# Kernel tuning notes

Measured on AMD Instinct MI355X. Metric: run time of the kernel, lower is better.

Reference implementation:

```python
import jax, jax.numpy as jnp
import numpy as np

H = 512      # hidden_size
R = 47       # response_size
TR = 2       # treat_size
B = 128
T = 512


def _uniform(key, shape, k):
    return jax.random.uniform(key, shape, jnp.float32, -k, k)


def setup_inputs() -> dict:
    key = jax.random.key(0)
    ks = jax.random.split(key, 20)
    kinit = 1.0 / np.sqrt(H)
    inp = {
        "x_r": jax.random.normal(ks[0], (B, T, R), jnp.float32),
        "x_t": jax.random.normal(ks[1], (B, T, TR), jnp.float32),
        # r_rnn: 2-layer LSTM, input size R+TR=49 (torch gate order i,f,g,o)
        "r_Wih0": _uniform(ks[2], (4 * H, R + TR), kinit),
        "r_Whh0": _uniform(ks[3], (4 * H, H), kinit),
        "r_b0": _uniform(ks[4], (4 * H,), kinit),  # b_ih + b_hh fused
        "r_Wih1": _uniform(ks[5], (4 * H, H), kinit),
        "r_Whh1": _uniform(ks[6], (4 * H, H), kinit),
        "r_b1": _uniform(ks[7], (4 * H,), kinit),
        # t_rnn: 2-layer LSTM, input size 2*R+TR=96
        "t_Wih0": _uniform(ks[8], (4 * H, 2 * R + TR), kinit),
        "t_Whh0": _uniform(ks[9], (4 * H, H), kinit),
        "t_b0": _uniform(ks[10], (4 * H,), kinit),
        "t_Wih1": _uniform(ks[11], (4 * H, H), kinit),
        "t_Whh1": _uniform(ks[12], (4 * H, H), kinit),
        "t_b1": _uniform(ks[13], (4 * H,), kinit),
        # output linears
        "Wr": _uniform(ks[14], (R, H), kinit),
        "br": _uniform(ks[15], (R,), kinit),
        "Wt": _uniform(ks[16], (TR, H), kinit),
        "bt": _uniform(ks[17], (TR,), kinit),
    }
    return inp


def _lstm_cell(x, h, c, Wih, Whh, b):
    gates = x @ Wih.T + h @ Whh.T + b          # [B, 4H]
    i, f, g, o = jnp.split(gates, 4, axis=-1)
    c = jax.nn.sigmoid(f) * c + jax.nn.sigmoid(i) * jnp.tanh(g)
    h = jax.nn.sigmoid(o) * jnp.tanh(c)
    return h, c


def reference(x_r, x_t, r_Wih0, r_Whh0, r_b0, r_Wih1, r_Whh1, r_b1,
              t_Wih0, t_Whh0, t_b0, t_Wih1, t_Whh1, t_b1, Wr, br, Wt, bt):
    b = x_r.shape[0]
    z = jnp.zeros((b, H), x_r.dtype)
    carry0 = (z, z, z, z, z, z, z, z)  # (h,c) for 2 layers of r_rnn and t_rnn

    def step(carry, rt):
        hr0, cr0, hr1, cr1, ht0, ct0, ht1, ct1 = carry
        r, t = rt
        r_input = jnp.concatenate([r, t], axis=-1)          # [B, 49]
        hr0, cr0 = _lstm_cell(r_input, hr0, cr0, r_Wih0, r_Whh0, r_b0)
        hr1, cr1 = _lstm_cell(hr0, hr1, cr1, r_Wih1, r_Whh1, r_b1)
        r_out = hr1 @ Wr.T + br                             # [B, 47]
        t_input = jnp.concatenate([r_input, r_out], axis=-1)  # [B, 96]
        ht0, ct0 = _lstm_cell(t_input, ht0, ct0, t_Wih0, t_Whh0, t_b0)
        ht1, ct1 = _lstm_cell(ht0, ht1, ct1, t_Wih1, t_Whh1, t_b1)
        t_out = ht1 @ Wt.T + bt                             # [B, 2]
        return (hr0, cr0, hr1, cr1, ht0, ct0, ht1, ct1), (r_out, t_out)

    xs = (jnp.swapaxes(x_r, 0, 1), jnp.swapaxes(x_t, 0, 1))  # time-major [T,B,.]
    _, (r_seq, t_seq) = jax.lax.scan(step, carry0, xs)
    # back to batch-first, like the module's final permute(1,0,2)
    return jnp.swapaxes(r_seq, 0, 1), jnp.swapaxes(t_seq, 0, 1)
```

## Files before the change

### kernel.cpp

```cpp
#include <hip/hip_runtime.h>


typedef _Float16 half_t;
typedef _Float16 half8 __attribute__((ext_vector_type(8)));
typedef float floatx4 __attribute__((ext_vector_type(4)));
typedef unsigned long long ull_t;

#define OFF_W0 0
#define OFF_W1 131072
#define OFF_W2 1179648
#define OFF_W3 2228224
#define OFF_W4 3276800
#define OFF_W5 3407872
#define OFF_W6 3538944
#define OFF_W7 4587520
#define OFF_W8 5636096
#define OFF_W9 6684672
#define OFF_W10 6709248
#define W_TOTAL 6717440
#define H_BASE  6717440
#define RO_BASE 7241728
#define HALF_TOTAL 7258112
#define STATE_BYTE_OFF (H_BASE * 2)
#define C_BYTE_OFF (HALF_TOTAL * 2)
#define BAR_BYTE_OFF 15564800
#define X16_BYTE_OFF (BAR_BYTE_OFF + 4096)
#define WS_NEED_X16 ((unsigned long long)X16_BYTE_OFF + 8388608ull)
#define STATE_BYTES (X16_BYTE_OFF - STATE_BYTE_OFF)

#define NBLK 256
#define TOUT_BASE (128 * 512 * 47)

__device__ __forceinline__ floatx4 mfma16(half8 a, half8 b, floatx4 c) {
  return __builtin_amdgcn_mfma_f32_16x16x32_f16(a, b, c, 0, 0, 0);
}
__device__ __forceinline__ float fast_sig(float x) {
  x = fminf(fmaxf(x, -30.f), 30.f);
  float e = __expf(-x);
  return __builtin_amdgcn_rcpf(1.f + e);
}
__device__ __forceinline__ float fast_tanh(float x) {
  x = fminf(fmaxf(x, -15.f), 15.f);
  float e = __expf(-2.f * x);
  return (1.f - e) * __builtin_amdgcn_rcpf(1.f + e);
}

template <int N>
__device__ __forceinline__ void coh_stage(half8 (&bb)[N], const half_t* p) {
#pragma unroll
  for (int ks = 0; ks < N; ++ks)
    asm volatile("global_load_dwordx4 %0, %1, off sc0 sc1"
                 : "=v"(bb[ks]) : "v"(p + ks * 32));
}
__device__ __forceinline__ void drain_vm() {
  asm volatile("s_waitcnt vmcnt(0)" ::: "memory");
  __builtin_amdgcn_sched_barrier(0);
}
__device__ __forceinline__ void store_h4_coh(half_t* p, half_t h0, half_t h1,
                                             half_t h2, half_t h3) {
  union { ull_t u; _Float16 h[4]; } x;
  x.h[0] = h0; x.h[1] = h1; x.h[2] = h2; x.h[3] = h3;
  __hip_atomic_store((ull_t*)p, x.u, __ATOMIC_RELAXED,
                     __HIP_MEMORY_SCOPE_AGENT);
}
template <int PACE>
__device__ __forceinline__ void poll_llc(const unsigned* p, unsigned target) {
  for (;;) {
    unsigned v;
    asm volatile("global_load_dword %0, %1, off sc0 sc1\ns_waitcnt vmcnt(0)"
                 : "=v"(v) : "v"(p));
    if (v >= target) return;
    __builtin_amdgcn_s_sleep(PACE);
  }
}

__device__ __forceinline__ void slab_issue(half8 (&tmp)[4],
                                           const half_t* __restrict__ src,
                                           int tid) {
#pragma unroll
  for (int j = 0; j < 4; ++j) {
    const int u = tid + j * 256;
    asm volatile("global_load_dwordx4 %0, %1, off sc0 sc1"
                 : "=v"(tmp[j]) : "v"(src + (u >> 6) * 512 + (u & 63) * 8));
  }
}
__device__ __forceinline__ void slab_write(char* base, const half8 (&tmp)[4],
                                           int tid) {
#pragma unroll
  for (int j = 0; j < 4; ++j) {
    const int u = tid + j * 256;
    const int row = u >> 6, seg = u & 63;
    *(half8*)(base + row * 1024 + ((seg * 16) ^ ((row & 7) << 4))) = tmp[j];
  }
}

template <int NT, int NSEG, int LDW>
__device__ __forceinline__ void gemm_lb(const half_t* __restrict__ W,
                                        const int* wrow, const char* ldsb,
                                        int lk, int q, int l15,
                                        floatx4 (&acc)[NT]) {
  const int bbase = l15 * 1024;
  const int bxor = (l15 & 7) << 4;
#pragma unroll
  for (int ks = 0; ks < NSEG; ++ks) {
    const int kb = ks * 32 + lk;
    half8 b = *(const half8*)(ldsb + bbase + ((q * 16 + ks * 64) ^ bxor));
#pragma unroll
    for (int n = 0; n < NT; ++n) {
      half8 a = *(const half8*)(W + (long)(wrow[n] + l15) * LDW + kb);
      acc[n] = mfma16(a, b, acc[n]);
    }
  }
}

template <int NT, int NSEG, int LDW>
__device__ __forceinline__ void gemm_regB(const half_t* __restrict__ W,
                                          const int* wrow,
                                          const half8 (&bb)[NSEG], int lk,
                                          int l15, floatx4 (&acc)[NT]) {
#pragma unroll
  for (int ks = 0; ks < NSEG; ++ks) {
    const int kb = ks * 32 + lk;
#pragma unroll
    for (int n = 0; n < NT; ++n) {
      half8 a = *(const half8*)(W + (long)(wrow[n] + l15) * LDW + kb);
      acc[n] = mfma16(a, bb[ks], acc[n]);
    }
  }
}

__device__ __forceinline__ void gemm_x16(const half_t* __restrict__ W,
                                         const int* wrow,
                                         const half_t* __restrict__ xb, int lk,
                                         int l15, floatx4 (&acc)[4]) {
#pragma unroll
  for (int ks = 0; ks < 2; ++ks) {
    const int kb = ks * 32 + lk;
    half8 b = *(const half8*)(xb + kb);
#pragma unroll
    for (int n = 0; n < 4; ++n) {
      half8 a = *(const half8*)(W + (long)(wrow[n] + l15) * 64 + kb);
      acc[n] = mfma16(a, b, acc[n]);
    }
  }
}
__device__ __forceinline__ void gemm_xf(const float* __restrict__ xr,
                                        const float* __restrict__ xt, int t,
                                        int batch, const half_t* __restrict__ W,
                                        const int* wrow, int lk, int l15,
                                        floatx4 (&acc)[4]) {
#pragma unroll
  for (int ks = 0; ks < 2; ++ks) {
    const int kb = ks * 32 + lk;
    half8 b;
    const long base = (long)batch * 512 + t;
#pragma unroll
    for (int j = 0; j < 8; ++j) {
      const int kk = kb + j;
      float f = 0.f;
      if (kk < 47) f = xr[base * 47 + kk];
      else if (kk < 49) f = xt[base * 2 + (kk - 47)];
      b[j] = (half_t)f;
    }
#pragma unroll
    for (int n = 0; n < 4; ++n) {
      half8 a = *(const half8*)(W + (long)(wrow[n] + l15) * 64 + kb);
      acc[n] = mfma16(a, b, acc[n]);
    }
  }
}

__device__ __forceinline__ void lstm_epi_sw(floatx4 (&acc)[4],
                                            const float* __restrict__ bias,
                                            float* __restrict__ cst,
                                            half_t* __restrict__ hdst,
                                            int batch, int hcol0) {
  const floatx4 bI = *(const floatx4*)(bias + hcol0);
  const floatx4 bF = *(const floatx4*)(bias + 512 + hcol0);
  const floatx4 bG = *(const floatx4*)(bias + 1024 + hcol0);
  const floatx4 bO = *(const floatx4*)(bias + 1536 + hcol0);
  const int off = batch * 512 + hcol0;
  floatx4 cold = *(floatx4*)(cst + off);
  floatx4 cn;
  half_t hn[4];
#pragma unroll
  for (int r = 0; r < 4; ++r) {
    const float gi = acc[0][r] + bI[r];
    const float gf = acc[1][r] + bF[r];
    const float gg = acc[2][r] + bG[r];
    const float go = acc[3][r] + bO[r];
    cn[r] = fast_sig(gf) * cold[r] + fast_sig(gi) * fast_tanh(gg);
    hn[r] = (half_t)(fast_sig(go) * fast_tanh(cn[r]));
  }
  *(floatx4*)(cst + off) = cn;
  store_h4_coh(hdst + off, hn[0], hn[1], hn[2], hn[3]);
}

__global__ __launch_bounds__(256, 1) void adrnn_persist(
    const float* __restrict__ xr, const float* __restrict__ xt,
    const float* __restrict__ b_r0, const float* __restrict__ b_r1,
    const float* __restrict__ b_t0, const float* __restrict__ b_t1,
    const float* __restrict__ brv, const float* __restrict__ btv,
    half_t* __restrict__ w16, float* __restrict__ cbase,
    float* __restrict__ out, unsigned* bar, const half_t* __restrict__ x16,
    int use_x16) {
  __shared__ half8 lds_v[2048];
  char* lds0 = (char*)lds_v;
  char* lds1 = lds0 + 16384;

  const int bid = blockIdx.x;
  const int tid = threadIdx.x;
  const int lane = tid & 63;
  const int w = tid >> 6;
  const int l15 = lane & 15;
  const int q = lane >> 4;
  const int lk = q * 8;
  half_t* H = w16 + H_BASE;
  half_t* RO = w16 + RO_BASE;
#define HB(cell, p) (H + (((cell)*2 + (p)) << 16))

  const int stage = (bid & 7) >> 1;
  const int hgHi = bid & 1;
  const int rr = bid >> 3;
  const int hgLo = rr >> 3;
  const int bg = rr & 7;
  const int hg = hgHi * 4 + hgLo;
  const int c0w = hg * 64 + w * 16;
  const int b0 = bg * 16;
  const int batch = b0 + l15;
  const int hcol0 = c0w + q * 4;
  const int sd = (stage == 0) ? 0 : (stage == 1) ? 1 : (stage == 2) ? 3 : 4;
  int wrow[4] = {c0w, 512 + c0w, 1024 + c0w, 1536 + c0w};
  const int flat = (hg * 8 + bg) * 4 + w;
  const bool is_spare = (stage == 0 && hg < 2 && flat < 32);

  unsigned* larr = bar + (bid & 7) * 32;
  unsigned* garr = bar + 256;
  unsigned* lgen = bar + 288 + (bid & 7) * 32;

  for (int k = 0; k < 517; ++k) {
    const int par = k & 1, pq = par ^ 1;
    const int t = k - sd;
    const bool valid = (t >= 0 && t < 512);

    if (valid) {
      half8 s0[4], s1[4];
      if (stage == 0) {
        slab_issue(s0, HB(0, pq) + b0 * 512, tid);
        drain_vm();
        slab_write(lds0, s0, tid);
      } else if (stage == 1) {
        slab_issue(s0, HB(0, pq) + b0 * 512, tid);
        slab_issue(s1, HB(1, pq) + b0 * 512, tid);
        drain_vm();
        slab_write(lds0, s0, tid);
        slab_write(lds1, s1, tid);
      } else if (stage == 2) {
        slab_issue(s0, HB(2, pq) + b0 * 512, tid);
        drain_vm();
        slab_write(lds0, s0, tid);
      } else {
        slab_issue(s0, HB(2, pq) + b0 * 512, tid);
        slab_issue(s1, HB(3, pq) + b0 * 512, tid);
        drain_vm();
        slab_write(lds0, s0, tid);
        slab_write(lds1, s1, tid);
      }
    }
    __syncthreads();

    if (valid) {
      floatx4 acc[4] = {};
      if (stage == 0) {
        if (use_x16)
          gemm_x16(w16 + OFF_W0, wrow, x16 + (long)t * 8192 + batch * 64, lk, l15, acc);
        else
          gemm_xf(xr, xt, t, batch, w16 + OFF_W0, wrow, lk, l15, acc);
        gemm_lb<4, 16, 512>(w16 + OFF_W1, wrow, lds0, lk, q, l15, acc);
        lstm_epi_sw(acc, b_r0, cbase + 0 * 65536, HB(0, par), batch, hcol0);
      } else if (stage == 1) {
        gemm_lb<4, 16, 512>(w16 + OFF_W2, wrow, lds0, lk, q, l15, acc);
        gemm_lb<4, 16, 512>(w16 + OFF_W3, wrow, lds1, lk, q, l15, acc);
        lstm_epi_sw(acc, b_r1, cbase + 1 * 65536, HB(1, par), batch, hcol0);
      } else if (stage == 2) {
        half8 bro[2];
        coh_stage<2>(bro, RO + pq * 8192 + batch * 64 + lk);
        drain_vm();
        if (use_x16)
          gemm_x16(w16 + OFF_W4, wrow, x16 + (long)t * 8192 + batch * 64, lk, l15, acc);
        else
          gemm_xf(xr, xt, t, batch, w16 + OFF_W4, wrow, lk, l15, acc);
        gemm_regB<4, 2, 64>(w16 + OFF_W5, wrow, bro, lk, l15, acc);
        gemm_lb<4, 16, 512>(w16 + OFF_W6, wrow, lds0, lk, q, l15, acc);
        lstm_epi_sw(acc, b_t0, cbase + 2 * 65536, HB(2, par), batch, hcol0);
      } else {
        gemm_lb<4, 16, 512>(w16 + OFF_W7, wrow, lds0, lk, q, l15, acc);
        gemm_lb<4, 16, 512>(w16 + OFF_W8, wrow, lds1, lk, q, l15, acc);
        lstm_epi_sw(acc, b_t1, cbase + 3 * 65536, HB(3, par), batch, hcol0);
      }
    }

    if (is_spare) {
      if (flat < 24) {
        const int tr = k - 2;
        if (tr >= 0 && tr < 512) {
          const int n = flat >> 3, btl = flat & 7;
          const int rb = btl * 16 + l15;
          half8 bs[16];
          coh_stage<16>(bs, HB(1, pq) + rb * 512 + lk);
          drain_vm();
          int wr1[1] = {n * 16};
          floatx4 accr[1] = {};
          gemm_regB<1, 16, 512>(w16 + OFF_W9, wr1, bs, lk, l15, accr);
          const int wc0 = n * 16 + q * 4;
          half_t ro4[4];
#pragma unroll
          for (int r = 0; r < 4; ++r) {
            const int wc = wc0 + r;
            float v = 0.f;
            if (wc < 47) {
              v = accr[0][r] + brv[wc];
              out[((long)rb * 512 + tr) * 47 + wc] = v;
            }
            ro4[r] = (half_t)v;
          }
          store_h4_coh(RO + par * 8192 + rb * 64 + wc0, ro4[0], ro4[1], ro4[2], ro4[3]);
        }
      } else {
        const int tt = k - 5;
        if (tt >= 0 && tt < 512) {
          const int btl = flat - 24;
          const int rb = btl * 16 + l15;
          half8 bs[16];
          coh_stage<16>(bs, HB(3, pq) + rb * 512 + lk);
          drain_vm();
          int wt1[1] = {0};
          floatx4 accw[1] = {};
          gemm_regB<1, 16, 512>(w16 + OFF_W10, wt1, bs, lk, l15, accw);
          if (q == 0) {
#pragma unroll
            for (int r = 0; r < 2; ++r)
              out[TOUT_BASE + ((long)rb * 512 + tt) * 2 + r] = accw[0][r] + btv[r];
          }
        }
      }
    }

    asm volatile("s_waitcnt vmcnt(0)" ::: "memory");
    __syncthreads();
    if (tid == 0) {
      const unsigned ku = (unsigned)k + 1u;
      (void)__hip_atomic_fetch_add(larr, 1u, __ATOMIC_RELAXED,
                                   __HIP_MEMORY_SCOPE_AGENT);
      if (bid < 8) {
        poll_llc<1>(larr, 32u * ku);
        (void)__hip_atomic_fetch_add(garr, 1u, __ATOMIC_RELAXED,
                                     __HIP_MEMORY_SCOPE_AGENT);
        poll_llc<1>(garr, 8u * ku);
        (void)__hip_atomic_fetch_add(lgen, 1u, __ATOMIC_RELAXED,
                                     __HIP_MEMORY_SCOPE_AGENT);
      } else {
        poll_llc<3>(lgen, ku);
      }
    }
    __syncthreads();
    asm volatile("" ::: "memory");
  }
#undef HB
}

__global__ __launch_bounds__(256) void conv_w(
    const float* __restrict__ rWih0, const float* __restrict__ rWhh0,
    const float* __restrict__ rWih1, const float* __restrict__ rWhh1,
    const float* __restrict__ tWih0, const float* __restrict__ tWhh0,
    const float* __restrict__ tWih1, const float* __restrict__ tWhh1,
    const float* __restrict__ Wr, const float* __restrict__ Wt,
    half_t* __restrict__ w16) {
  const int idx = blockIdx.x * 256 + threadIdx.x;
  if (idx >= W_TOTAL) return;
  float v = 0.f;
  if (idx < OFF_W1) {
    int n = idx >> 6, kk = idx & 63;
    if (kk < 49) v = rWih0[n * 49 + kk];
  } else if (idx < OFF_W2) {
    int r = idx - OFF_W1; v = rWhh0[r];
  } else if (idx < OFF_W3) {
    int r = idx - OFF_W2; v = rWih1[r];
  } else if (idx < OFF_W4) {
    int r = idx - OFF_W3; v = rWhh1[r];
  } else if (idx < OFF_W5) {
    int r = idx - OFF_W4; int n = r >> 6, kk = r & 63;
    if (kk < 49) v = tWih0[n * 96 + kk];
  } else if (idx < OFF_W6) {
    int r = idx - OFF_W5; int n = r >> 6, kk = r & 63;
    if (kk < 47) v = tWih0[n * 96 + 49 + kk];
  } else if (idx < OFF_W7) {
    int r = idx - OFF_W6; v = tWhh0[r];
  } else if (idx < OFF_W8) {
    int r = idx - OFF_W7; v = tWih1[r];
  } else if (idx < OFF_W9) {
    int r = idx - OFF_W8; v = tWhh1[r];
  } else if (idx < OFF_W10) {
    int r = idx - OFF_W9; int n = r >> 9, kk = r & 511;
    if (n < 47) v = Wr[n * 512 + kk];
  } else {
    int r = idx - OFF_W10; int n = r >> 9, kk = r & 511;
    if (n < 2) v = Wt[n * 512 + kk];
  }
  w16[idx] = (half_t)v;
}

__global__ __launch_bounds__(256) void conv_x(const float* __restrict__ xr,
                                              const float* __restrict__ xt,
                                              half_t* __restrict__ x16) {
  const int idx = blockIdx.x * 256 + threadIdx.x;
  if (idx >= 512 * 128 * 64) return;
  const int kk = idx & 63;
  const int row = (idx >> 6) & 127;
  const int t = idx >> 13;
  float v = 0.f;
  if (kk < 47) v = xr[(row * 512 + t) * 47 + kk];
  else if (kk < 49) v = xt[(row * 512 + t) * 2 + (kk - 47)];
  x16[idx] = (half_t)v;
}

extern "C" void kernel_launch(void* const* d_in, const int* in_sizes, int n_in,
                              void* d_out, int out_size, void* d_ws,
                              size_t ws_size, hipStream_t stream) {
  const float* xr = (const float*)d_in[0];
  const float* xt = (const float*)d_in[1];
  const float* rWih0 = (const float*)d_in[2];
  const float* rWhh0 = (const float*)d_in[3];
  const float* r_b0 = (const float*)d_in[4];
  const float* rWih1 = (const float*)d_in[5];
  const float* rWhh1 = (const float*)d_in[6];
  const float* r_b1 = (const float*)d_in[7];
  const float* tWih0 = (const float*)d_in[8];
  const float* tWhh0 = (const float*)d_in[9];
  const float* t_b0 = (const float*)d_in[10];
  const float* tWih1 = (const float*)d_in[11];
  const float* tWhh1 = (const float*)d_in[12];
  const float* t_b1 = (const float*)d_in[13];
  const float* Wr = (const float*)d_in[14];
  const float* br = (const float*)d_in[15];
  const float* Wt = (const float*)d_in[16];
  const float* bt = (const float*)d_in[17];

  half_t* w16 = (half_t*)d_ws;
  float* cbase = (float*)((char*)d_ws + C_BYTE_OFF);
  unsigned* bar = (unsigned*)((char*)d_ws + BAR_BYTE_OFF);
  half_t* x16 = (half_t*)((char*)d_ws + X16_BYTE_OFF);
  float* out = (float*)d_out;
  int use_x16 = (ws_size >= WS_NEED_X16) ? 1 : 0;

  (void)hipMemsetAsync((char*)d_ws + STATE_BYTE_OFF, 0, STATE_BYTES, stream);

  conv_w<<<(W_TOTAL + 255) / 256, 256, 0, stream>>>(
      rWih0, rWhh0, rWih1, rWhh1, tWih0, tWhh0, tWih1, tWhh1, Wr, Wt, w16);
  if (use_x16)
    conv_x<<<(512 * 128 * 64) / 256, 256, 0, stream>>>(xr, xt, x16);

  adrnn_persist<<<NBLK, 256, 0, stream>>>(xr, xt, r_b0, r_b1, t_b0, t_b1, br,
                                          bt, w16, cbase, out, bar, x16,
                                          use_x16);
}
```

Measured before the change: 9.214 ms.

## Remap blocks so most hidden-state traffic stays XCD-local; publish cross-stage h via LLC

Changes the block-to-work mapping so the producer and consumer of each LSTM layer's hidden state share the same XCD (bid&1 parity). Those local exchanges now use non-system-coherent loads and plain stores. Only the cross-stage h (layer 0 to layer 1, t-layer 0 to t-layer 1) is written a second time to a separate global buffer with LLC-coherent stores. The output-projection spare work moves to stage-1 and stage-3 blocks that read locally, aiming to cut the latency of coherent memory traffic on every timestep, at the cost of a duplicate h store and some reliance on same-XCD L2 visibility.

```diff
diff --git a/kernel.cpp b/kernel.cpp
--- a/kernel.cpp
+++ b/kernel.cpp
@@ -20,10 +20,11 @@
 #define W_TOTAL 6717440
 #define H_BASE  6717440
 #define RO_BASE 7241728
-#define HALF_TOTAL 7258112
+#define HG_BASE 7258112
+#define HALF_END 7520256
 #define STATE_BYTE_OFF (H_BASE * 2)
-#define C_BYTE_OFF (HALF_TOTAL * 2)
-#define BAR_BYTE_OFF 15564800
+#define C_BYTE_OFF (HALF_END * 2)
+#define BAR_BYTE_OFF (C_BYTE_OFF + 1048576)
 #define X16_BYTE_OFF (BAR_BYTE_OFF + 4096)
 #define WS_NEED_X16 ((unsigned long long)X16_BYTE_OFF + 8388608ull)
 #define STATE_BYTES (X16_BYTE_OFF - STATE_BYTE_OFF)
@@ -46,22 +47,26 @@
 }
 
 template <int N>
-__device__ __forceinline__ void coh_stage(half8 (&bb)[N], const half_t* p) {
+__device__ __forceinline__ void burst_g(half8 (&bb)[N], const half_t* p) {
 #pragma unroll
   for (int ks = 0; ks < N; ++ks)
     asm volatile("global_load_dwordx4 %0, %1, off sc0 sc1"
                  : "=v"(bb[ks]) : "v"(p + ks * 32));
 }
+template <int N>
+__device__ __forceinline__ void burst_l(half8 (&bb)[N], const half_t* p) {
+#pragma unroll
+  for (int ks = 0; ks < N; ++ks)
+    asm volatile("global_load_dwordx4 %0, %1, off sc0"
+                 : "=v"(bb[ks]) : "v"(p + ks * 32));
+}
 __device__ __forceinline__ void drain_vm() {
   asm volatile("s_waitcnt vmcnt(0)" ::: "memory");
   __builtin_amdgcn_sched_barrier(0);
 }
-__device__ __forceinline__ void store_h4_coh(half_t* p, half_t h0, half_t h1,
-                                             half_t h2, half_t h3) {
-  union { ull_t u; _Float16 h[4]; } x;
-  x.h[0] = h0; x.h[1] = h1; x.h[2] = h2; x.h[3] = h3;
-  __hip_atomic_store((ull_t*)p, x.u, __ATOMIC_RELAXED,
-                     __HIP_MEMORY_SCOPE_AGENT);
+__device__ __forceinline__ void store8_llc(half_t* p, ull_t v) {
+  asm volatile("global_store_dwordx2 %0, %1, off sc0 sc1"
+               :: "v"(p), "v"(v) : "memory");
 }
 template <int PACE>
 __device__ __forceinline__ void poll_llc(const unsigned* p, unsigned target) {
@@ -74,14 +79,19 @@
   }
 }
 
+template <int LLC>
 __device__ __forceinline__ void slab_issue(half8 (&tmp)[4],
                                            const half_t* __restrict__ src,
                                            int tid) {
 #pragma unroll
   for (int j = 0; j < 4; ++j) {
     const int u = tid + j * 256;
-    asm volatile("global_load_dwordx4 %0, %1, off sc0 sc1"
-                 : "=v"(tmp[j]) : "v"(src + (u >> 6) * 512 + (u & 63) * 8));
+    if constexpr (LLC)
+      asm volatile("global_load_dwordx4 %0, %1, off sc0 sc1"
+                   : "=v"(tmp[j]) : "v"(src + (u >> 6) * 512 + (u & 63) * 8));
+    else
+      asm volatile("global_load_dwordx4 %0, %1, off sc0"
+                   : "=v"(tmp[j]) : "v"(src + (u >> 6) * 512 + (u & 63) * 8));
   }
 }
 __device__ __forceinline__ void slab_write(char* base, const half8 (&tmp)[4],
@@ -112,7 +122,6 @@
     }
   }
 }
-
 template <int NT, int NSEG, int LDW>
 __device__ __forceinline__ void gemm_regB(const half_t* __restrict__ W,
                                           const int* wrow,
@@ -128,7 +137,6 @@
     }
   }
 }
-
 __device__ __forceinline__ void gemm_x16(const half_t* __restrict__ W,
                                          const int* wrow,
                                          const half_t* __restrict__ xb, int lk,
@@ -170,11 +178,11 @@
   }
 }
 
-__device__ __forceinline__ void lstm_epi_sw(floatx4 (&acc)[4],
-                                            const float* __restrict__ bias,
-                                            float* __restrict__ cst,
-                                            half_t* __restrict__ hdst,
-                                            int batch, int hcol0) {
+__device__ __forceinline__ void lstm_epi(floatx4 (&acc)[4],
+                                         const float* __restrict__ bias,
+                                         float* __restrict__ cst,
+                                         half_t* __restrict__ hld,
+                                         half_t* hgd, int batch, int hcol0) {
   const floatx4 bI = *(const floatx4*)(bias + hcol0);
   const floatx4 bF = *(const floatx4*)(bias + 512 + hcol0);
   const floatx4 bG = *(const floatx4*)(bias + 1024 + hcol0);
@@ -182,7 +190,7 @@
   const int off = batch * 512 + hcol0;
   floatx4 cold = *(floatx4*)(cst + off);
   floatx4 cn;
-  half_t hn[4];
+  union { ull_t u; _Float16 h[4]; } pk;
 #pragma unroll
   for (int r = 0; r < 4; ++r) {
     const float gi = acc[0][r] + bI[r];
@@ -190,10 +198,11 @@
     const float gg = acc[2][r] + bG[r];
     const float go = acc[3][r] + bO[r];
     cn[r] = fast_sig(gf) * cold[r] + fast_sig(gi) * fast_tanh(gg);
-    hn[r] = (half_t)(fast_sig(go) * fast_tanh(cn[r]));
+    pk.h[r] = (half_t)(fast_sig(go) * fast_tanh(cn[r]));
   }
   *(floatx4*)(cst + off) = cn;
-  store_h4_coh(hdst + off, hn[0], hn[1], hn[2], hn[3]);
+  *(ull_t*)(hld + off) = pk.u;
+  if (hgd) store8_llc(hgd + off, pk.u);
 }
 
 __global__ __launch_bounds__(256, 1) void adrnn_persist(
@@ -215,24 +224,25 @@
   const int l15 = lane & 15;
   const int q = lane >> 4;
   const int lk = q * 8;
-  half_t* H = w16 + H_BASE;
+  half_t* HL = w16 + H_BASE;
   half_t* RO = w16 + RO_BASE;
-#define HB(cell, p) (H + (((cell)*2 + (p)) << 16))
+#define HLB(cell, s) (HL + (((cell)*2 + (s)) << 16))
+#define HG0(s) (w16 + HG_BASE + ((s) << 16))
+#define HG2(s) (w16 + HG_BASE + 131072 + ((s) << 16))
 
   const int stage = (bid & 7) >> 1;
-  const int hgHi = bid & 1;
-  const int rr = bid >> 3;
-  const int hgLo = rr >> 3;
-  const int bg = rr & 7;
-  const int hg = hgHi * 4 + hgLo;
+  const int p = bid & 1;
+  const int u = bid >> 3;
+  const int hg = u >> 2;
+  const int bgHi = u & 3;
+  const int bg = bgHi * 2 + p;
   const int c0w = hg * 64 + w * 16;
   const int b0 = bg * 16;
   const int batch = b0 + l15;
   const int hcol0 = c0w + q * 4;
   const int sd = (stage == 0) ? 0 : (stage == 1) ? 1 : (stage == 2) ? 3 : 4;
   int wrow[4] = {c0w, 512 + c0w, 1024 + c0w, 1536 + c0w};
-  const int flat = (hg * 8 + bg) * 4 + w;
-  const bool is_spare = (stage == 0 && hg < 2 && flat < 32);
+  const int flat = u * 4 + w;
 
   unsigned* larr = bar + (bid & 7) * 32;
   unsigned* garr = bar + 256;
@@ -246,22 +256,22 @@
     if (valid) {
       half8 s0[4], s1[4];
       if (stage == 0) {
-        slab_issue(s0, HB(0, pq) + b0 * 512, tid);
+        slab_issue<0>(s0, HLB(0, pq) + b0 * 512, tid);
         drain_vm();
         slab_write(lds0, s0, tid);
       } else if (stage == 1) {
-        slab_issue(s0, HB(0, pq) + b0 * 512, tid);
-        slab_issue(s1, HB(1, pq) + b0 * 512, tid);
+        slab_issue<1>(s0, HG0(pq) + b0 * 512, tid);
+        slab_issue<0>(s1, HLB(1, pq) + b0 * 512, tid);
         drain_vm();
         slab_write(lds0, s0, tid);
         slab_write(lds1, s1, tid);
       } else if (stage == 2) {
-        slab_issue(s0, HB(2, pq) + b0 * 512, tid);
+        slab_issue<0>(s0, HLB(2, pq) + b0 * 512, tid);
         drain_vm();
         slab_write(lds0, s0, tid);
       } else {
-        slab_issue(s0, HB(2, pq) + b0 * 512, tid);
-        slab_issue(s1, HB(3, pq) + b0 * 512, tid);
+        slab_issue<1>(s0, HG2(pq) + b0 * 512, tid);
+        slab_issue<0>(s1, HLB(3, pq) + b0 * 512, tid);
         drain_vm();
         slab_write(lds0, s0, tid);
         slab_write(lds1, s1, tid);
@@ -277,14 +287,14 @@
         else
           gemm_xf(xr, xt, t, batch, w16 + OFF_W0, wrow, lk, l15, acc);
         gemm_lb<4, 16, 512>(w16 + OFF_W1, wrow, lds0, lk, q, l15, acc);
-        lstm_epi_sw(acc, b_r0, cbase + 0 * 65536, HB(0, par), batch, hcol0);
+        lstm_epi(acc, b_r0, cbase + 0 * 65536, HLB(0, par), HG0(par), batch, hcol0);
       } else if (stage == 1) {
         gemm_lb<4, 16, 512>(w16 + OFF_W2, wrow, lds0, lk, q, l15, acc);
         gemm_lb<4, 16, 512>(w16 + OFF_W3, wrow, lds1, lk, q, l15, acc);
-        lstm_epi_sw(acc, b_r1, cbase + 1 * 65536, HB(1, par), batch, hcol0);
+        lstm_epi(acc, b_r1, cbase + 1 * 65536, HLB(1, par), nullptr, batch, hcol0);
       } else if (stage == 2) {
         half8 bro[2];
-        coh_stage<2>(bro, RO + pq * 8192 + batch * 64 + lk);
+        burst_g<2>(bro, RO + pq * 8192 + batch * 64 + lk);
         drain_vm();
         if (use_x16)
           gemm_x16(w16 + OFF_W4, wrow, x16 + (long)t * 8192 + batch * 64, lk, l15, acc);
@@ -292,56 +302,55 @@
           gemm_xf(xr, xt, t, batch, w16 + OFF_W4, wrow, lk, l15, acc);
         gemm_regB<4, 2, 64>(w16 + OFF_W5, wrow, bro, lk, l15, acc);
         gemm_lb<4, 16, 512>(w16 + OFF_W6, wrow, lds0, lk, q, l15, acc);
-        lstm_epi_sw(acc, b_t0, cbase + 2 * 65536, HB(2, par), batch, hcol0);
+        lstm_epi(acc, b_t0, cbase + 2 * 65536, HLB(2, par), HG2(par), batch, hcol0);
       } else {
         gemm_lb<4, 16, 512>(w16 + OFF_W7, wrow, lds0, lk, q, l15, acc);
         gemm_lb<4, 16, 512>(w16 + OFF_W8, wrow, lds1, lk, q, l15, acc);
-        lstm_epi_sw(acc, b_t1, cbase + 3 * 65536, HB(3, par), batch, hcol0);
+        lstm_epi(acc, b_t1, cbase + 3 * 65536, HLB(3, par), nullptr, batch, hcol0);
       }
     }
 
-    if (is_spare) {
-      if (flat < 24) {
-        const int tr = k - 2;
-        if (tr >= 0 && tr < 512) {
-          const int n = flat >> 3, btl = flat & 7;
-          const int rb = btl * 16 + l15;
-          half8 bs[16];
-          coh_stage<16>(bs, HB(1, pq) + rb * 512 + lk);
-          drain_vm();
-          int wr1[1] = {n * 16};
-          floatx4 accr[1] = {};
-          gemm_regB<1, 16, 512>(w16 + OFF_W9, wr1, bs, lk, l15, accr);
-          const int wc0 = n * 16 + q * 4;
-          half_t ro4[4];
-#pragma unroll
-          for (int r = 0; r < 4; ++r) {
-            const int wc = wc0 + r;
-            float v = 0.f;
-            if (wc < 47) {
-              v = accr[0][r] + brv[wc];
-              out[((long)rb * 512 + tr) * 47 + wc] = v;
-            }
-            ro4[r] = (half_t)v;
+    if (stage == 1 && flat < 12) {
+      const int tr = k - 2;
+      if (tr >= 0 && tr < 512) {
+        const int n = flat >> 2;
+        const int btl = (flat & 3) * 2 + p;
+        const int rb = btl * 16 + l15;
+        half8 bs[16];
+        burst_l<16>(bs, HLB(1, pq) + rb * 512 + lk);
+        drain_vm();
+        int wr1[1] = {n * 16};
+        floatx4 accr[1] = {};
+        gemm_regB<1, 16, 512>(w16 + OFF_W9, wr1, bs, lk, l15, accr);
+        const int wc0 = n * 16 + q * 4;
+        union { ull_t u2; _Float16 h[4]; } rp;
+#pragma unroll
+        for (int r = 0; r < 4; ++r) {
+          const int wc = wc0 + r;
+          float v = 0.f;
+          if (wc < 47) {
+            v = accr[0][r] + brv[wc];
+            out[((long)rb * 512 + tr) * 47 + wc] = v;
           }
-          store_h4_coh(RO + par * 8192 + rb * 64 + wc0, ro4[0], ro4[1], ro4[2], ro4[3]);
+          rp.h[r] = (half_t)v;
         }
-      } else {
-        const int tt = k - 5;
-        if (tt >= 0 && tt < 512) {
-          const int btl = flat - 24;
-          const int rb = btl * 16 + l15;
-          half8 bs[16];
-          coh_stage<16>(bs, HB(3, pq) + rb * 512 + lk);
-          drain_vm();
-          int wt1[1] = {0};
-          floatx4 accw[1] = {};
-          gemm_regB<1, 16, 512>(w16 + OFF_W10, wt1, bs, lk, l15, accw);
-          if (q == 0) {
-#pragma unroll
-            for (int r = 0; r < 2; ++r)
-              out[TOUT_BASE + ((long)rb * 512 + tt) * 2 + r] = accw[0][r] + btv[r];
-          }
+        store8_llc(RO + par * 8192 + rb * 64 + wc0, rp.u2);
+      }
+    } else if (stage == 3 && flat < 4) {
+      const int tt = k - 5;
+      if (tt >= 0 && tt < 512) {
+        const int btl = flat * 2 + p;
+        const int rb = btl * 16 + l15;
+        half8 bs[16];
+        burst_l<16>(bs, HLB(3, pq) + rb * 512 + lk);
+        drain_vm();
+        int wt1[1] = {0};
+        floatx4 accw[1] = {};
+        gemm_regB<1, 16, 512>(w16 + OFF_W10, wt1, bs, lk, l15, accw);
+        if (q == 0) {
+#pragma unroll
+          for (int r = 0; r < 2; ++r)
+            out[TOUT_BASE + ((long)rb * 512 + tt) * 2 + r] = accw[0][r] + btv[r];
         }
       }
     }
@@ -366,7 +375,9 @@
     __syncthreads();
     asm volatile("" ::: "memory");
   }
-#undef HB
+#undef HLB
+#undef HG0
+#undef HG2
 }
 
 __global__ __launch_bounds__(256) void conv_w(
```

After: 11.74 ms. 1.27x slower.

## Halve persistent blocks, double per-wave gate tiles, fold output heads into stages

Applied to the files above, without the earlier changes.

Cuts the persistent grid from 256 to 128 blocks. Each wave now computes two 16-column hidden tiles per gate, eight accumulators instead of four, so the LDS-staged hidden state is reused across twice as many weight rows. The separate spare blocks that computed the r_out and t_out linears are gone. Those projections now run in existing stage-1 and stage-3 blocks, which reuse the h already in LDS instead of reloading it from global memory. The barrier arrival count is lowered to match, which reduces synchronisation fan-in, at the cost of more serial MFMA and weight-load work per block each step.

```diff
diff --git a/kernel.cpp b/kernel.cpp
--- a/kernel.cpp
+++ b/kernel.cpp
@@ -28,7 +28,7 @@
 #define WS_NEED_X16 ((unsigned long long)X16_BYTE_OFF + 8388608ull)
 #define STATE_BYTES (X16_BYTE_OFF - STATE_BYTE_OFF)
 
-#define NBLK 256
+#define NBLK 128
 #define TOUT_BASE (128 * 512 * 47)
 
 __device__ __forceinline__ floatx4 mfma16(half8 a, half8 b, floatx4 c) {
@@ -46,7 +46,7 @@
 }
 
 template <int N>
-__device__ __forceinline__ void coh_stage(half8 (&bb)[N], const half_t* p) {
+__device__ __forceinline__ void burst_g(half8 (&bb)[N], const half_t* p) {
 #pragma unroll
   for (int ks = 0; ks < N; ++ks)
     asm volatile("global_load_dwordx4 %0, %1, off sc0 sc1"
@@ -56,12 +56,8 @@
   asm volatile("s_waitcnt vmcnt(0)" ::: "memory");
   __builtin_amdgcn_sched_barrier(0);
 }
-__device__ __forceinline__ void store_h4_coh(half_t* p, half_t h0, half_t h1,
-                                             half_t h2, half_t h3) {
-  union { ull_t u; _Float16 h[4]; } x;
-  x.h[0] = h0; x.h[1] = h1; x.h[2] = h2; x.h[3] = h3;
-  __hip_atomic_store((ull_t*)p, x.u, __ATOMIC_RELAXED,
-                     __HIP_MEMORY_SCOPE_AGENT);
+__device__ __forceinline__ void store_h4_coh(half_t* p, ull_t v) {
+  __hip_atomic_store((ull_t*)p, v, __ATOMIC_RELAXED, __HIP_MEMORY_SCOPE_AGENT);
 }
 template <int PACE>
 __device__ __forceinline__ void poll_llc(const unsigned* p, unsigned target) {
@@ -73,6 +69,10 @@
     __builtin_amdgcn_s_sleep(PACE);
   }
 }
+__device__ __forceinline__ void cnt_add(unsigned* p) {
+  (void)__hip_atomic_fetch_add(p, 1u, __ATOMIC_RELAXED,
+                               __HIP_MEMORY_SCOPE_AGENT);
+}
 
 __device__ __forceinline__ void slab_issue(half8 (&tmp)[4],
                                            const half_t* __restrict__ src,
@@ -112,7 +112,6 @@
     }
   }
 }
-
 template <int NT, int NSEG, int LDW>
 __device__ __forceinline__ void gemm_regB(const half_t* __restrict__ W,
                                           const int* wrow,
@@ -128,27 +127,28 @@
     }
   }
 }
-
+template <int NT>
 __device__ __forceinline__ void gemm_x16(const half_t* __restrict__ W,
                                          const int* wrow,
                                          const half_t* __restrict__ xb, int lk,
-                                         int l15, floatx4 (&acc)[4]) {
+                                         int l15, floatx4 (&acc)[NT]) {
 #pragma unroll
   for (int ks = 0; ks < 2; ++ks) {
     const int kb = ks * 32 + lk;
     half8 b = *(const half8*)(xb + kb);
 #pragma unroll
-    for (int n = 0; n < 4; ++n) {
+    for (int n = 0; n < NT; ++n) {
       half8 a = *(const half8*)(W + (long)(wrow[n] + l15) * 64 + kb);
       acc[n] = mfma16(a, b, acc[n]);
     }
   }
 }
+template <int NT>
 __device__ __forceinline__ void gemm_xf(const float* __restrict__ xr,
                                         const float* __restrict__ xt, int t,
                                         int batch, const half_t* __restrict__ W,
                                         const int* wrow, int lk, int l15,
-                                        floatx4 (&acc)[4]) {
+                                        floatx4 (&acc)[NT]) {
 #pragma unroll
   for (int ks = 0; ks < 2; ++ks) {
     const int kb = ks * 32 + lk;
@@ -163,37 +163,41 @@
       b[j] = (half_t)f;
     }
 #pragma unroll
-    for (int n = 0; n < 4; ++n) {
+    for (int n = 0; n < NT; ++n) {
       half8 a = *(const half8*)(W + (long)(wrow[n] + l15) * 64 + kb);
       acc[n] = mfma16(a, b, acc[n]);
     }
   }
 }
 
-__device__ __forceinline__ void lstm_epi_sw(floatx4 (&acc)[4],
-                                            const float* __restrict__ bias,
-                                            float* __restrict__ cst,
-                                            half_t* __restrict__ hdst,
-                                            int batch, int hcol0) {
-  const floatx4 bI = *(const floatx4*)(bias + hcol0);
-  const floatx4 bF = *(const floatx4*)(bias + 512 + hcol0);
-  const floatx4 bG = *(const floatx4*)(bias + 1024 + hcol0);
-  const floatx4 bO = *(const floatx4*)(bias + 1536 + hcol0);
-  const int off = batch * 512 + hcol0;
-  floatx4 cold = *(floatx4*)(cst + off);
-  floatx4 cn;
-  half_t hn[4];
-#pragma unroll
-  for (int r = 0; r < 4; ++r) {
-    const float gi = acc[0][r] + bI[r];
-    const float gf = acc[1][r] + bF[r];
-    const float gg = acc[2][r] + bG[r];
-    const float go = acc[3][r] + bO[r];
-    cn[r] = fast_sig(gf) * cold[r] + fast_sig(gi) * fast_tanh(gg);
-    hn[r] = (half_t)(fast_sig(go) * fast_tanh(cn[r]));
-  }
-  *(floatx4*)(cst + off) = cn;
-  store_h4_coh(hdst + off, hn[0], hn[1], hn[2], hn[3]);
+__device__ __forceinline__ void lstm_epi2(floatx4 (&acc)[8],
+                                          const float* __restrict__ bias,
+                                          float* __restrict__ cst,
+                                          half_t* __restrict__ hdst,
+                                          int batch, int c0w, int q) {
+#pragma unroll
+  for (int j = 0; j < 2; ++j) {
+    const int hcol0 = c0w + j * 16 + q * 4;
+    const floatx4 bI = *(const floatx4*)(bias + hcol0);
+    const floatx4 bF = *(const floatx4*)(bias + 512 + hcol0);
+    const floatx4 bG = *(const floatx4*)(bias + 1024 + hcol0);
+    const floatx4 bO = *(const floatx4*)(bias + 1536 + hcol0);
+    const int off = batch * 512 + hcol0;
+    floatx4 cold = *(floatx4*)(cst + off);
+    floatx4 cn;
+    union { ull_t u; _Float16 h[4]; } pk;
+#pragma unroll
+    for (int r = 0; r < 4; ++r) {
+      const float gi = acc[0 + j][r] + bI[r];
+      const float gf = acc[2 + j][r] + bF[r];
+      const float gg = acc[4 + j][r] + bG[r];
+      const float go = acc[6 + j][r] + bO[r];
+      cn[r] = fast_sig(gf) * cold[r] + fast_sig(gi) * fast_tanh(gg);
+      pk.h[r] = (half_t)(fast_sig(go) * fast_tanh(cn[r]));
+    }
+    *(floatx4*)(cst + off) = cn;
+    store_h4_coh(hdst + off, pk.u);
+  }
 }
 
 __global__ __launch_bounds__(256, 1) void adrnn_persist(
@@ -224,15 +228,19 @@
   const int rr = bid >> 3;
   const int hgLo = rr >> 3;
   const int bg = rr & 7;
-  const int hg = hgHi * 4 + hgLo;
-  const int c0w = hg * 64 + w * 16;
+  const int hg = hgHi * 2 + hgLo;
+  const int c0w = hg * 128 + w * 32;
   const int b0 = bg * 16;
   const int batch = b0 + l15;
-  const int hcol0 = c0w + q * 4;
   const int sd = (stage == 0) ? 0 : (stage == 1) ? 1 : (stage == 2) ? 3 : 4;
-  int wrow[4] = {c0w, 512 + c0w, 1024 + c0w, 1536 + c0w};
-  const int flat = (hg * 8 + bg) * 4 + w;
-  const bool is_spare = (stage == 0 && hg < 2 && flat < 32);
+  int wrow[8];
+#pragma unroll
+  for (int g = 0; g < 4; ++g) {
+    wrow[g * 2 + 0] = g * 512 + c0w;
+    wrow[g * 2 + 1] = g * 512 + c0w + 16;
+  }
+  const bool do_rout = (stage == 1 && hg == 0 && w < 3);
+  const bool do_tout = (stage == 3 && hg == 0 && w == 0);
 
   unsigned* larr = bar + (bid & 7) * 32;
   unsigned* garr = bar + 256;
@@ -243,7 +251,7 @@
     const int t = k - sd;
     const bool valid = (t >= 0 && t < 512);
 
-    if (valid) {
+    {
       half8 s0[4], s1[4];
       if (stage == 0) {
         slab_issue(s0, HB(0, pq) + b0 * 512, tid);
@@ -270,78 +278,69 @@
     __syncthreads();
 
     if (valid) {
-      floatx4 acc[4] = {};
+      floatx4 acc[8] = {};
       if (stage == 0) {
         if (use_x16)
-          gemm_x16(w16 + OFF_W0, wrow, x16 + (long)t * 8192 + batch * 64, lk, l15, acc);
+          gemm_x16<8>(w16 + OFF_W0, wrow, x16 + (long)t * 8192 + batch * 64, lk, l15, acc);
         else
-          gemm_xf(xr, xt, t, batch, w16 + OFF_W0, wrow, lk, l15, acc);
-        gemm_lb<4, 16, 512>(w16 + OFF_W1, wrow, lds0, lk, q, l15, acc);
-        lstm_epi_sw(acc, b_r0, cbase + 0 * 65536, HB(0, par), batch, hcol0);
+          gemm_xf<8>(xr, xt, t, batch, w16 + OFF_W0, wrow, lk, l15, acc);
+        gemm_lb<8, 16, 512>(w16 + OFF_W1, wrow, lds0, lk, q, l15, acc);
+        lstm_epi2(acc, b_r0, cbase + 0 * 65536, HB(0, par), batch, c0w, q);
       } else if (stage == 1) {
-        gemm_lb<4, 16, 512>(w16 + OFF_W2, wrow, lds0, lk, q, l15, acc);
-        gemm_lb<4, 16, 512>(w16 + OFF_W3, wrow, lds1, lk, q, l15, acc);
-        lstm_epi_sw(acc, b_r1, cbase + 1 * 65536, HB(1, par), batch, hcol0);
+        gemm_lb<8, 16, 512>(w16 + OFF_W2, wrow, lds0, lk, q, l15, acc);
+        gemm_lb<8, 16, 512>(w16 + OFF_W3, wrow, lds1, lk, q, l15, acc);
+        lstm_epi2(acc, b_r1, cbase + 1 * 65536, HB(1, par), batch, c0w, q);
       } else if (stage == 2) {
         half8 bro[2];
-        coh_stage<2>(bro, RO + pq * 8192 + batch * 64 + lk);
+        burst_g<2>(bro, RO + pq * 8192 + batch * 64 + lk);
         drain_vm();
         if (use_x16)
-          gemm_x16(w16 + OFF_W4, wrow, x16 + (long)t * 8192 + batch * 64, lk, l15, acc);
+          gemm_x16<8>(w16 + OFF_W4, wrow, x16 + (long)t * 8192 + batch * 64, lk, l15, acc);
         else
-          gemm_xf(xr, xt, t, batch, w16 + OFF_W4, wrow, lk, l15, acc);
-        gemm_regB<4, 2, 64>(w16 + OFF_W5, wrow, bro, lk, l15, acc);
-        gemm_lb<4, 16, 512>(w16 + OFF_W6, wrow, lds0, lk, q, l15, acc);
-        lstm_epi_sw(acc, b_t0, cbase + 2 * 65536, HB(2, par), batch, hcol0);
+          gemm_xf<8>(xr, xt, t, batch, w16 + OFF_W4, wrow, lk, l15, acc);
+        gemm_regB<8, 2, 64>(w16 + OFF_W5, wrow, bro, lk, l15, acc);
+        gemm_lb<8, 16, 512>(w16 + OFF_W6, wrow, lds0, lk, q, l15, acc);
+        lstm_epi2(acc, b_t0, cbase + 2 * 65536, HB(2, par), batch, c0w, q);
       } else {
-        gemm_lb<4, 16, 512>(w16 + OFF_W7, wrow, lds0, lk, q, l15, acc);
-        gemm_lb<4, 16, 512>(w16 + OFF_W8, wrow, lds1, lk, q, l15, acc);
-        lstm_epi_sw(acc, b_t1, cbase + 3 * 65536, HB(3, par), batch, hcol0);
+        gemm_lb<8, 16, 512>(w16 + OFF_W7, wrow, lds0, lk, q, l15, acc);
+        gemm_lb<8, 16, 512>(w16 + OFF_W8, wrow, lds1, lk, q, l15, acc);
+        lstm_epi2(acc, b_t1, cbase + 3 * 65536, HB(3, par), batch, c0w, q);
       }
     }
 
-    if (is_spare) {
-      if (flat < 24) {
-        const int tr = k - 2;
-        if (tr >= 0 && tr < 512) {
-          const int n = flat >> 3, btl = flat & 7;
-          const int rb = btl * 16 + l15;
-          half8 bs[16];
-          coh_stage<16>(bs, HB(1, pq) + rb * 512 + lk);
-          drain_vm();
-          int wr1[1] = {n * 16};
-          floatx4 accr[1] = {};
-          gemm_regB<1, 16, 512>(w16 + OFF_W9, wr1, bs, lk, l15, accr);
-          const int wc0 = n * 16 + q * 4;
-          half_t ro4[4];
-#pragma unroll
-          for (int r = 0; r < 4; ++r) {
-            const int wc = wc0 + r;
-            float v = 0.f;
-            if (wc < 47) {
-              v = accr[0][r] + brv[wc];
-              out[((long)rb * 512 + tr) * 47 + wc] = v;
-            }
-            ro4[r] = (half_t)v;
+    if (do_rout) {
+      const int tro = k - 2;
+      if (tro >= 0 && tro < 512) {
+        int wr1[1] = {w * 16};
+        floatx4 accr[1] = {};
+        gemm_lb<1, 16, 512>(w16 + OFF_W9, wr1, lds1, lk, q, l15, accr);
+        const int rb = b0 + l15;
+        const int wc0 = w * 16 + q * 4;
+        union { ull_t u2; _Float16 h[4]; } rp;
+#pragma unroll
+        for (int r = 0; r < 4; ++r) {
+          const int wc = wc0 + r;
+          float v = 0.f;
+          if (wc < 47) {
+            v = accr[0][r] + brv[wc];
+            out[((long)rb * 512 + tro) * 47 + wc] = v;
           }
-          store_h4_coh(RO + par * 8192 + rb * 64 + wc0, ro4[0], ro4[1], ro4[2], ro4[3]);
+          rp.h[r] = (half_t)v;
         }
-      } else {
-        const int tt = k - 5;
-        if (tt >= 0 && tt < 512) {
-          const int btl = flat - 24;
-          const int rb = btl * 16 + l15;
-          half8 bs[16];
-          coh_stage<16>(bs, HB(3, pq) + rb * 512 + lk);
-          drain_vm();
-          int wt1[1] = {0};
-          floatx4 accw[1] = {};
-          gemm_regB<1, 16, 512>(w16 + OFF_W10, wt1, bs, lk, l15, accw);
-          if (q == 0) {
-#pragma unroll
-            for (int r = 0; r < 2; ++r)
-              out[TOUT_BASE + ((long)rb * 512 + tt) * 2 + r] = accw[0][r] + btv[r];
-          }
+        store_h4_coh(RO + par * 8192 + rb * 64 + wc0, rp.u2);
+      }
+    }
+    if (do_tout) {
+      const int tto = k - 5;
+      if (tto >= 0 && tto < 512) {
+        int wt1[1] = {0};
+        floatx4 accw[1] = {};
+        gemm_lb<1, 16, 512>(w16 + OFF_W10, wt1, lds1, lk, q, l15, accw);
+        if (q == 0) {
+          const int rb = b0 + l15;
+#pragma unroll
+          for (int r = 0; r < 2; ++r)
+            out[TOUT_BASE + ((long)rb * 512 + tto) * 2 + r] = accw[0][r] + btv[r];
         }
       }
     }
@@ -350,15 +349,12 @@
     __syncthreads();
     if (tid == 0) {
       const unsigned ku = (unsigned)k + 1u;
-      (void)__hip_atomic_fetch_add(larr, 1u, __ATOMIC_RELAXED,
-                                   __HIP_MEMORY_SCOPE_AGENT);
+      cnt_add(larr);
       if (bid < 8) {
-        poll_llc<1>(larr, 32u * ku);
-        (void)__hip_atomic_fetch_add(garr, 1u, __ATOMIC_RELAXED,
-                                     __HIP_MEMORY_SCOPE_AGENT);
+        poll_llc<1>(larr, 16u * ku);
+        cnt_add(garr);
         poll_llc<1>(garr, 8u * ku);
-        (void)__hip_atomic_fetch_add(lgen, 1u, __ATOMIC_RELAXED,
-                                     __HIP_MEMORY_SCOPE_AGENT);
+        cnt_add(lgen);
       } else {
         poll_llc<3>(lgen, ku);
       }
```

Measured after the change: 18.38 ms. 2x slower.
